# Optimization experiments

Hardware: AMD Instinct MI355X
Metric: run time of the kernel (lower is better)

The kernel has to match this reference:

```python
import jax, jax.numpy as jnp
import numpy as np

D_MODEL = 1024
N_HEADS = 16
D_HEAD = D_MODEL // N_HEADS
B, T = 2, 2048


def setup_inputs() -> dict:
    key = jax.random.key(0)
    ks = jax.random.split(key, 6)
    scale = 1.0 / np.sqrt(D_MODEL)
    x = jax.random.normal(ks[0], (B, T, D_MODEL), dtype=jnp.float32)
    mask = jax.random.randint(ks[1], (1, 1, T, T), 0, 2, dtype=jnp.int32)
    Wqkv = jax.random.normal(ks[2], (D_MODEL, 3 * D_MODEL), dtype=jnp.float32) * scale
    bqkv = jnp.zeros((3 * D_MODEL,), dtype=jnp.float32)
    Wproj = jax.random.normal(ks[3], (D_MODEL, D_MODEL), dtype=jnp.float32) * scale
    bproj = jnp.zeros((D_MODEL,), dtype=jnp.float32)
    return {"x": x, "mask": mask, "Wqkv": Wqkv, "bqkv": bqkv,
            "Wproj": Wproj, "bproj": bproj}


def reference(x, mask, Wqkv, bqkv, Wproj, bproj):
    Bx, Tx, C = x.shape
    qkv = x @ Wqkv + bqkv                      # [B,T,3C]
    q, k, v = jnp.split(qkv, 3, axis=-1)       # each [B,T,C]

    def heads(t):  # [B,T,C] -> [B,H,T,dh]
        return t.reshape(Bx, Tx, N_HEADS, D_HEAD).transpose(0, 2, 1, 3)

    q, k, v = heads(q), heads(k), heads(v)
    att = jnp.einsum('bhqd,bhkd->bhqk', q, k) / jnp.sqrt(jnp.float32(D_HEAD))
    att = jnp.where(mask == 1, -jnp.inf, att)
    att = jax.nn.softmax(att, axis=-1)
    out = jnp.einsum('bhqk,bhkd->bhqd', att, v)  # [B,H,T,dh]
    out = out.transpose(0, 2, 1, 3).reshape(Bx, Tx, C)
    return out @ Wproj + bproj
```

## Files before the change

kernel.cpp:

```cpp
#include <hip/hip_runtime.h>
#include <hip/hip_bf16.h>

#define T_DIM 2048
#define C_DIM 1024
#define NHEAD 16
#define DHEAD 64

typedef __attribute__((ext_vector_type(8))) short s16x8;
typedef __attribute__((ext_vector_type(4))) short s16x4;
typedef __attribute__((ext_vector_type(4))) float f32x4;
typedef __attribute__((ext_vector_type(4))) unsigned short u16x4;

static __device__ __forceinline__ unsigned short f2bfu(float f){
  __hip_bfloat16 h = __float2bfloat16(f);
  unsigned short u;
  __builtin_memcpy(&u, &h, 2);
  return u;
}

static __device__ __forceinline__ f32x4 MFMA16(s16x8 a, s16x8 b, f32x4 c){
  return __builtin_amdgcn_mfma_f32_16x16x32_bf16(a, b, c, 0, 0, 0);
}

__global__ __launch_bounds__(256) void cvt_bf16_kernel(const float* __restrict__ in,
                                                       unsigned short* __restrict__ out, int n4){
  int i = blockIdx.x*256 + threadIdx.x;
  if (i < n4){
    float4 v = reinterpret_cast<const float4*>(in)[i];
    u16x4 o;
    o.x = f2bfu(v.x); o.y = f2bfu(v.y); o.z = f2bfu(v.z); o.w = f2bfu(v.w);
    reinterpret_cast<u16x4*>(out)[i] = o;
  }
}

__global__ __launch_bounds__(256) void transpose_cvt_kernel(const float* __restrict__ src,
                                                            unsigned short* __restrict__ dst,
                                                            int K, int N){
  __shared__ unsigned short tile[64][65];
  int n0 = blockIdx.x*64, k0 = blockIdx.y*64;
  int tid = threadIdx.x;
  #pragma unroll
  for (int i=0;i<16;i++){
    int e = i*256 + tid; int r = e>>6, c = e&63;
    tile[r][c] = f2bfu(src[(size_t)(k0+r)*N + n0 + c]);
  }
  __syncthreads();
  #pragma unroll
  for (int i=0;i<16;i++){
    int e = i*256 + tid; int r = e>>6, c = e&63;
    dst[(size_t)(n0+r)*K + k0 + c] = tile[c][r];
  }
}

__global__ __launch_bounds__(256) void mask_bits_kernel(const int* __restrict__ m,
                                                        unsigned int* __restrict__ bits){
  int i = blockIdx.x*256 + threadIdx.x;
  unsigned long long b = __ballot(m[i] == 1);
  int lane = threadIdx.x & 63;
  if (lane == 0)  bits[i>>5] = (unsigned int)b;
  if (lane == 32) bits[i>>5] = (unsigned int)(b>>32);
}

__global__ __launch_bounds__(256) void transpose_v_kernel(const unsigned short* __restrict__ v,
                                                          unsigned short* __restrict__ vt){
  __shared__ unsigned short tile[64][65];
  int bh = blockIdx.y;
  int t0 = blockIdx.x*64;
  const unsigned short* src = v + (size_t)bh*T_DIM*DHEAD;
  unsigned short* dst = vt + (size_t)bh*T_DIM*DHEAD;
  int tid = threadIdx.x;
  #pragma unroll
  for (int i=0;i<16;i++){
    int e = i*256+tid; int r = e>>6, c = e&63;
    tile[r][c] = src[(size_t)(t0+r)*DHEAD + c];
  }
  __syncthreads();
  #pragma unroll
  for (int i=0;i<16;i++){
    int e = i*256+tid; int r = e>>6, c = e&63;
    dst[(size_t)r*T_DIM + t0 + c] = tile[c][r];
  }
}

template<int MODE>
__global__ __launch_bounds__(256) void gemm_kernel(const unsigned short* __restrict__ A,
    const unsigned short* __restrict__ Bt, const float* __restrict__ bias,
    unsigned short* __restrict__ qo, unsigned short* __restrict__ ko,
    unsigned short* __restrict__ vo, float* __restrict__ out)
{
  const int K = 1024;
  __shared__ __align__(16) unsigned short As[128][72];
  __shared__ __align__(16) unsigned short Bs[128][72];
  int tid = threadIdx.x;
  int lane = tid & 63, wave = tid >> 6;
  int m0 = blockIdx.y*128, n0 = blockIdx.x*128;
  int wm = (wave>>1)*64, wn = (wave&1)*64;
  int lr = lane & 15, lg = lane >> 4;
  f32x4 acc[4][4];
  #pragma unroll
  for (int i=0;i<4;i++){
    #pragma unroll
    for (int j=0;j<4;j++){
      #pragma unroll
      for (int r=0;r<4;r++) acc[i][j][r] = 0.f;
    }
  }
  for (int kt=0; kt<K; kt+=64){
    #pragma unroll
    for (int it=0; it<4; it++){
      int t = it*256 + tid;
      int r = t>>3, ch = (t&7)*8;
      *reinterpret_cast<s16x8*>(&As[r][ch]) =
          *reinterpret_cast<const s16x8*>(A + (size_t)(m0+r)*K + kt + ch);
      *reinterpret_cast<s16x8*>(&Bs[r][ch]) =
          *reinterpret_cast<const s16x8*>(Bt + (size_t)(n0+r)*K + kt + ch);
    }
    __syncthreads();
    #pragma unroll
    for (int kk=0; kk<2; kk++){
      s16x8 av[4], bv[4];
      #pragma unroll
      for (int i=0;i<4;i++){
        av[i] = *reinterpret_cast<const s16x8*>(&As[wm + i*16 + lr][kk*32 + lg*8]);
        bv[i] = *reinterpret_cast<const s16x8*>(&Bs[wn + i*16 + lr][kk*32 + lg*8]);
      }
      #pragma unroll
      for (int i=0;i<4;i++){
        #pragma unroll
        for (int j=0;j<4;j++)
          acc[i][j] = MFMA16(av[i], bv[j], acc[i][j]);
      }
    }
    __syncthreads();
  }
  #pragma unroll
  for (int j=0;j<4;j++){
    int n = n0 + wn + j*16 + lr;
    float bvl = bias[n];
    #pragma unroll
    for (int i=0;i<4;i++){
      #pragma unroll
      for (int r=0;r<4;r++){
        int m = m0 + wm + i*16 + lg*4 + r;
        float val = acc[i][j][r] + bvl;
        if (MODE == 0){
          int which = n >> 10, c = n & 1023;
          int h = c >> 6, d = c & 63;
          int b = m >> 11, t = m & 2047;
          size_t idx = ((size_t)((b*NHEAD + h)*T_DIM + t))*DHEAD + d;
          unsigned short us = f2bfu(val);
          if (which == 0) qo[idx] = us;
          else if (which == 1) ko[idx] = us;
          else vo[idx] = us;
        } else {
          out[(size_t)m*C_DIM + n] = val;
        }
      }
    }
  }
}

__global__ __launch_bounds__(256) void attn_kernel(const unsigned short* __restrict__ q,
    const unsigned short* __restrict__ k, const unsigned short* __restrict__ vt,
    const unsigned int* __restrict__ mbits, unsigned short* __restrict__ aout)
{
  __shared__ __align__(16) unsigned short Ks[64][72];
  __shared__ __align__(16) unsigned short Vs[64][72];
  __shared__ __align__(16) unsigned short Ps[4][16][72];
  int bh = blockIdx.y;
  int q0 = blockIdx.x*64;
  int tid = threadIdx.x, lane = tid&63, wave = tid>>6;
  int lr = lane&15, lg = lane>>4;
  const unsigned short* qp = q  + (size_t)bh*T_DIM*DHEAD;
  const unsigned short* kp = k  + (size_t)bh*T_DIM*DHEAD;
  const unsigned short* vp = vt + (size_t)bh*T_DIM*DHEAD;
  int qw = q0 + wave*16;
  s16x8 qf[2];
  #pragma unroll
  for (int kk=0;kk<2;kk++)
    qf[kk] = *reinterpret_cast<const s16x8*>(qp + (size_t)(qw+lr)*DHEAD + kk*32 + lg*8);
  f32x4 o[4];
  #pragma unroll
  for (int cb=0;cb<4;cb++){
    #pragma unroll
    for (int r=0;r<4;r++) o[cb][r]=0.f;
  }
  float m = -1e30f, l = 0.f;
  const unsigned int* mptr = mbits + (size_t)(qw + lr)*(T_DIM/32);

  for (int k0=0; k0<T_DIM; k0+=64){
    #pragma unroll
    for (int it=0; it<2; it++){
      int t = it*256 + tid;
      int r = t>>3, ch = (t&7)*8;
      *reinterpret_cast<s16x8*>(&Ks[r][ch]) =
          *reinterpret_cast<const s16x8*>(kp + (size_t)(k0+r)*DHEAD + ch);
      *reinterpret_cast<s16x8*>(&Vs[r][ch]) =
          *reinterpret_cast<const s16x8*>(vp + (size_t)r*T_DIM + k0 + ch);
    }
    __syncthreads();
    f32x4 st[4];
    #pragma unroll
    for (int cb=0;cb<4;cb++){
      f32x4 a;
      #pragma unroll
      for (int r=0;r<4;r++) a[r]=0.f;
      #pragma unroll
      for (int kk=0;kk<2;kk++){
        s16x8 kf = *reinterpret_cast<const s16x8*>(&Ks[cb*16 + lr][kk*32 + lg*8]);
        a = MFMA16(kf, qf[kk], a);
      }
      st[cb] = a;
    }
    unsigned mw0 = mptr[(k0>>5)];
    unsigned mw1 = mptr[(k0>>5)+1];
    #pragma unroll
    for (int cb=0;cb<4;cb++){
      unsigned msel = (cb<2) ? mw0 : mw1;
      unsigned ms = msel >> ((cb&1)*16 + lg*4);
      #pragma unroll
      for (int r=0;r<4;r++){
        float val = st[cb][r]*0.125f;
        st[cb][r] = ((ms>>r)&1u) ? -1e30f : val;
      }
    }
    float pmax = st[0][0];
    #pragma unroll
    for (int cb=0;cb<4;cb++){
      #pragma unroll
      for (int r=0;r<4;r++) pmax = fmaxf(pmax, st[cb][r]);
    }
    pmax = fmaxf(pmax, __shfl_xor(pmax, 16));
    pmax = fmaxf(pmax, __shfl_xor(pmax, 32));
    float mnew = fmaxf(m, pmax);
    float corr = __expf(m - mnew);
    m = mnew;
    float rs = 0.f;
    #pragma unroll
    for (int cb=0;cb<4;cb++){
      #pragma unroll
      for (int r=0;r<4;r++){
        float p = __expf(st[cb][r] - mnew);
        st[cb][r] = p;
        rs += p;
      }
    }
    rs += __shfl_xor(rs, 16);
    rs += __shfl_xor(rs, 32);
    l = l*corr + rs;
    float corrO[4];
    #pragma unroll
    for (int r=0;r<4;r++) corrO[r] = __shfl(corr, lg*4 + r);
    #pragma unroll
    for (int cb=0;cb<4;cb++){
      #pragma unroll
      for (int r=0;r<4;r++) o[cb][r] *= corrO[r];
    }
    #pragma unroll
    for (int cb=0;cb<4;cb++){
      s16x4 pk;
      #pragma unroll
      for (int r=0;r<4;r++) pk[r] = (short)f2bfu(st[cb][r]);
      *reinterpret_cast<s16x4*>(&Ps[wave][lr][cb*16 + lg*4]) = pk;
    }
    s16x8 pf[2];
    #pragma unroll
    for (int kk=0;kk<2;kk++)
      pf[kk] = *reinterpret_cast<const s16x8*>(&Ps[wave][lr][kk*32 + lg*8]);
    #pragma unroll
    for (int cb=0;cb<4;cb++){
      #pragma unroll
      for (int kk=0;kk<2;kk++){
        s16x8 vf = *reinterpret_cast<const s16x8*>(&Vs[cb*16 + lr][kk*32 + lg*8]);
        o[cb] = MFMA16(pf[kk], vf, o[cb]);
      }
    }
    __syncthreads();
  }
  int b = bh >> 4, h = bh & 15;
  float inv = l > 0.f ? 1.f/l : 0.f;
  #pragma unroll
  for (int r=0;r<4;r++){
    float invO = __shfl(inv, lg*4 + r);
    int row = b*T_DIM + qw + lg*4 + r;
    #pragma unroll
    for (int cb=0;cb<4;cb++){
      int d = cb*16 + lr;
      aout[(size_t)row*C_DIM + h*DHEAD + d] = f2bfu(o[cb][r]*invO);
    }
  }
}

extern "C" void kernel_launch(void* const* d_in, const int* in_sizes, int n_in,
                              void* d_out, int out_size, void* d_ws, size_t ws_size,
                              hipStream_t stream){
  const float* x     = (const float*)d_in[0];
  const int*   mask  = (const int*)d_in[1];
  const float* Wqkv  = (const float*)d_in[2];
  const float* bqkv  = (const float*)d_in[3];
  const float* Wproj = (const float*)d_in[4];
  const float* bproj = (const float*)d_in[5];
  float* out = (float*)d_out;
  char* ws = (char*)d_ws;
  const size_t MB = (size_t)1<<20;
  unsigned short* xb     = (unsigned short*)(ws + 0*MB);
  unsigned short* wqkvT  = (unsigned short*)(ws + 8*MB);
  unsigned short* wprojT = (unsigned short*)(ws + 14*MB);
  unsigned int*   mbits  = (unsigned int*)(ws + 16*MB);
  unsigned short* qb     = (unsigned short*)(ws + 17*MB);
  unsigned short* kb     = (unsigned short*)(ws + 25*MB);
  unsigned short* vb     = (unsigned short*)(ws + 33*MB);
  unsigned short* vtb    = (unsigned short*)(ws + 41*MB);
  unsigned short* aout   = xb;

  cvt_bf16_kernel<<<dim3(4096), dim3(256), 0, stream>>>(x, xb, (2*2048*1024)/4);
  transpose_cvt_kernel<<<dim3(48,16), dim3(256), 0, stream>>>(Wqkv, wqkvT, 1024, 3072);
  transpose_cvt_kernel<<<dim3(16,16), dim3(256), 0, stream>>>(Wproj, wprojT, 1024, 1024);
  mask_bits_kernel<<<dim3((2048*2048)/256), dim3(256), 0, stream>>>(mask, mbits);
  gemm_kernel<0><<<dim3(24,32), dim3(256), 0, stream>>>(xb, wqkvT, bqkv, qb, kb, vb, nullptr);
  transpose_v_kernel<<<dim3(32,32), dim3(256), 0, stream>>>(vb, vtb);
  attn_kernel<<<dim3(32,32), dim3(256), 0, stream>>>(qb, kb, vtb, mbits, aout);
  gemm_kernel<1><<<dim3(8,32), dim3(256), 0, stream>>>(aout, wprojT, bproj, nullptr, nullptr, nullptr, out);
}
```

Before: 256.7 us.

## Use direct global-to-LDS loads with XOR swizzle in GEMM; drop LDS staging in attention

The GEMM kernel now fills its tiles with global_load_lds (direct DMA into LDS) in an unpadded XOR-swizzled layout, and the fragment reads are adjusted to match. This avoids staging through registers and avoids bank conflicts without padding. The attention kernel no longer stages K and V in shared memory: each wave loads its MFMA fragments straight from global memory, which removes both block barriers, but the four waves now fetch the same K/V data redundantly and rely on the cache. Softmax is rewritten to use exp2f with log2(e) folded into the scale factor.

```diff
diff --git a/kernel.cpp b/kernel.cpp
--- a/kernel.cpp
+++ b/kernel.cpp
@@ -10,6 +10,9 @@
 typedef __attribute__((ext_vector_type(4))) short s16x4;
 typedef __attribute__((ext_vector_type(4))) float f32x4;
 typedef __attribute__((ext_vector_type(4))) unsigned short u16x4;
+
+typedef __attribute__((address_space(3))) unsigned short lds_us;
+typedef const __attribute__((address_space(1))) void glb_v;
 
 static __device__ __forceinline__ unsigned short f2bfu(float f){
   __hip_bfloat16 h = __float2bfloat16(f);
@@ -89,13 +92,18 @@
     unsigned short* __restrict__ vo, float* __restrict__ out)
 {
   const int K = 1024;
-  __shared__ __align__(16) unsigned short As[128][72];
-  __shared__ __align__(16) unsigned short Bs[128][72];
+  __shared__ __align__(16) unsigned short As[128*64];
+  __shared__ __align__(16) unsigned short Bs[128*64];
   int tid = threadIdx.x;
   int lane = tid & 63, wave = tid >> 6;
   int m0 = blockIdx.y*128, n0 = blockIdx.x*128;
   int wm = (wave>>1)*64, wn = (wave&1)*64;
   int lr = lane & 15, lg = lane >> 4;
+  int srow  = wave*8 + (lane>>3);
+  int sslot = (lane&7) ^ (lane>>3);
+  const unsigned short* Asrc = A  + (size_t)(m0+srow)*K + sslot*8;
+  const unsigned short* Bsrc = Bt + (size_t)(n0+srow)*K + sslot*8;
+  unsigned ldsoff = (unsigned)(wave*512 + lane*8);
   f32x4 acc[4][4];
   #pragma unroll
   for (int i=0;i<4;i++){
@@ -107,13 +115,11 @@
   }
   for (int kt=0; kt<K; kt+=64){
     #pragma unroll
-    for (int it=0; it<4; it++){
-      int t = it*256 + tid;
-      int r = t>>3, ch = (t&7)*8;
-      *reinterpret_cast<s16x8*>(&As[r][ch]) =
-          *reinterpret_cast<const s16x8*>(A + (size_t)(m0+r)*K + kt + ch);
-      *reinterpret_cast<s16x8*>(&Bs[r][ch]) =
-          *reinterpret_cast<const s16x8*>(Bt + (size_t)(n0+r)*K + kt + ch);
+    for (int i=0;i<4;i++){
+      __builtin_amdgcn_global_load_lds((glb_v*)(Asrc + (size_t)i*32*K + kt),
+                                       (lds_us*)(As + ldsoff + i*2048), 16, 0, 0);
+      __builtin_amdgcn_global_load_lds((glb_v*)(Bsrc + (size_t)i*32*K + kt),
+                                       (lds_us*)(Bs + ldsoff + i*2048), 16, 0, 0);
     }
     __syncthreads();
     #pragma unroll
@@ -121,8 +127,8 @@
       s16x8 av[4], bv[4];
       #pragma unroll
       for (int i=0;i<4;i++){
-        av[i] = *reinterpret_cast<const s16x8*>(&As[wm + i*16 + lr][kk*32 + lg*8]);
-        bv[i] = *reinterpret_cast<const s16x8*>(&Bs[wn + i*16 + lr][kk*32 + lg*8]);
+        av[i] = *reinterpret_cast<const s16x8*>(&As[(wm+i*16+lr)*64 + (((kk*4+lg)^(lr&7))<<3)]);
+        bv[i] = *reinterpret_cast<const s16x8*>(&Bs[(wn+i*16+lr)*64 + (((kk*4+lg)^(lr&7))<<3)]);
       }
       #pragma unroll
       for (int i=0;i<4;i++){
@@ -164,8 +170,6 @@
     const unsigned short* __restrict__ k, const unsigned short* __restrict__ vt,
     const unsigned int* __restrict__ mbits, unsigned short* __restrict__ aout)
 {
-  __shared__ __align__(16) unsigned short Ks[64][72];
-  __shared__ __align__(16) unsigned short Vs[64][72];
   __shared__ __align__(16) unsigned short Ps[4][16][72];
   int bh = blockIdx.y;
   int q0 = blockIdx.x*64;
@@ -185,20 +189,11 @@
     #pragma unroll
     for (int r=0;r<4;r++) o[cb][r]=0.f;
   }
+  const float SC = 0.125f * 1.44269504f;
   float m = -1e30f, l = 0.f;
   const unsigned int* mptr = mbits + (size_t)(qw + lr)*(T_DIM/32);
 
   for (int k0=0; k0<T_DIM; k0+=64){
-    #pragma unroll
-    for (int it=0; it<2; it++){
-      int t = it*256 + tid;
-      int r = t>>3, ch = (t&7)*8;
-      *reinterpret_cast<s16x8*>(&Ks[r][ch]) =
-          *reinterpret_cast<const s16x8*>(kp + (size_t)(k0+r)*DHEAD + ch);
-      *reinterpret_cast<s16x8*>(&Vs[r][ch]) =
-          *reinterpret_cast<const s16x8*>(vp + (size_t)r*T_DIM + k0 + ch);
-    }
-    __syncthreads();
     f32x4 st[4];
     #pragma unroll
     for (int cb=0;cb<4;cb++){
@@ -207,7 +202,8 @@
       for (int r=0;r<4;r++) a[r]=0.f;
       #pragma unroll
       for (int kk=0;kk<2;kk++){
-        s16x8 kf = *reinterpret_cast<const s16x8*>(&Ks[cb*16 + lr][kk*32 + lg*8]);
+        s16x8 kf = *reinterpret_cast<const s16x8*>(
+            kp + (size_t)(k0 + cb*16 + lr)*DHEAD + kk*32 + lg*8);
         a = MFMA16(kf, qf[kk], a);
       }
       st[cb] = a;
@@ -220,7 +216,7 @@
       unsigned ms = msel >> ((cb&1)*16 + lg*4);
       #pragma unroll
       for (int r=0;r<4;r++){
-        float val = st[cb][r]*0.125f;
+        float val = st[cb][r]*SC;
         st[cb][r] = ((ms>>r)&1u) ? -1e30f : val;
       }
     }
@@ -233,14 +229,14 @@
     pmax = fmaxf(pmax, __shfl_xor(pmax, 16));
     pmax = fmaxf(pmax, __shfl_xor(pmax, 32));
     float mnew = fmaxf(m, pmax);
-    float corr = __expf(m - mnew);
+    float corr = exp2f(m - mnew);
     m = mnew;
     float rs = 0.f;
     #pragma unroll
     for (int cb=0;cb<4;cb++){
       #pragma unroll
       for (int r=0;r<4;r++){
-        float p = __expf(st[cb][r] - mnew);
+        float p = exp2f(st[cb][r] - mnew);
         st[cb][r] = p;
         rs += p;
       }
@@ -271,11 +267,11 @@
     for (int cb=0;cb<4;cb++){
       #pragma unroll
       for (int kk=0;kk<2;kk++){
-        s16x8 vf = *reinterpret_cast<const s16x8*>(&Vs[cb*16 + lr][kk*32 + lg*8]);
+        s16x8 vf = *reinterpret_cast<const s16x8*>(
+            vp + (size_t)(cb*16 + lr)*T_DIM + k0 + kk*32 + lg*8);
         o[cb] = MFMA16(pf[kk], vf, o[cb]);
       }
     }
-    __syncthreads();
   }
   int b = bh >> 4, h = bh & 15;
   float inv = l > 0.f ? 1.f/l : 0.f;
```

Result: slower. 410.2 us (+59.8%).
